# Performance work log

Measured on AMD Instinct MI355X. Metric: run time of the kernel, lower is better.

The kernel has to match this reference:

```python
import jax, jax.numpy as jnp
import numpy as np

MAX_CAV = 5


def setup_inputs() -> dict:
    key = jax.random.key(0)
    k1, k2, k3, k4, k5 = jax.random.split(key, 5)
    # ragged group lengths, each <= MAX_CAV, sum = 25
    record_len = jnp.array([3, 5, 2, 4, 1, 5, 3, 2], dtype=jnp.int32)
    N, C, H, W = 25, 256, 48, 176
    x = jax.random.normal(k1, (N, C, H, W), dtype=jnp.float32)
    W1 = jax.random.normal(k2, (MAX_CAV, 2 * MAX_CAV), dtype=jnp.float32) * 0.3
    W2 = jax.random.normal(k3, (MAX_CAV, MAX_CAV), dtype=jnp.float32) * 0.3
    conv_w = jax.random.normal(k4, (MAX_CAV,), dtype=jnp.float32) * 0.3
    conv_b = jax.random.normal(k5, (1,), dtype=jnp.float32) * 0.1
    return dict(x=x, record_len=record_len, W1=W1, W2=W2, conv_w=conv_w, conv_b=conv_b)


def _pad_regroup(x, record_len, max_cav):
    # scatter ragged tokens into a zero-padded [bs, max_cav, C, H, W] buffer
    N = x.shape[0]
    bs = record_len.shape[0]
    cum = jnp.cumsum(record_len)
    tok = jnp.arange(N)
    b = jnp.searchsorted(cum, tok, side='right')      # batch id per token
    slot = tok - (cum[b] - record_len[b])             # position within group
    padded = jnp.zeros((bs, max_cav) + x.shape[1:], x.dtype)
    return padded.at[b, slot].set(x)


def reference(x, record_len, W1, W2, conv_w, conv_b):
    padded = _pad_regroup(x, record_len, MAX_CAV)     # [bs, M, C, H, W]
    # AdaptiveAvg/MaxPool3d(1) over (C,H,W); padded slots are all-zero -> max=0
    x_avg = padded.mean(axis=(2, 3, 4))               # [bs, M]
    x_max = padded.max(axis=(2, 3, 4))                # [bs, M]
    x_sq = jnp.concatenate([x_avg, x_max], axis=1)    # [bs, 2M]
    gate = jax.nn.relu(jax.nn.sigmoid(x_sq @ W1.T) @ W2.T)  # [bs, M]
    scaled = padded * gate[:, :, None, None, None]
    # 1x1x1 Conv3d(M -> 1) == weighted sum over CAV axis + bias, then ReLU
    out = jax.nn.relu(jnp.einsum('m,bmchw->bchw', conv_w, scaled) + conv_b[0])
    return out
```

## Files before the change

### kernel.cpp

```cpp
#include <hip/hip_runtime.h>
#include <math.h>

#define CHW     2162688
#define V4      540672
#define NTOK    25
#define MAXCAV  5
#define NBATCH  8

#define BPT     64
#define V4_BLK  8448
#define ITERS   33

#define ABLKS   1056
#define CHUNK3  512

typedef float f32x4 __attribute__((ext_vector_type(4)));

__global__ __launch_bounds__(256) void k_reduce(const float4* __restrict__ x,
                                                float* __restrict__ psum,
                                                float* __restrict__ pmax) {
    const int tid = threadIdx.x;
    const int t   = blockIdx.y;
    const int blk = blockIdx.x;
    const long base = (long)t * V4 + (long)blk * V4_BLK;

    float s = 0.0f;
    float mx = -INFINITY;
    #pragma unroll 4
    for (int i = 0; i < ITERS; ++i) {
        float4 v = x[base + i * 256 + tid];
        s += (v.x + v.y) + (v.z + v.w);
        mx = fmaxf(mx, fmaxf(fmaxf(v.x, v.y), fmaxf(v.z, v.w)));
    }

    const int lane = tid & 63;
    const int wave = tid >> 6;
    #pragma unroll
    for (int off = 32; off > 0; off >>= 1) {
        s += __shfl_xor(s, off, 64);
        mx = fmaxf(mx, __shfl_xor(mx, off, 64));
    }
    __shared__ float rs[4], rm[4];
    if (lane == 0) { rs[wave] = s; rm[wave] = mx; }
    __syncthreads();
    if (tid == 0) {
        psum[t * BPT + blk] = rs[0] + rs[1] + rs[2] + rs[3];
        pmax[t * BPT + blk] = fmaxf(fmaxf(rm[0], rm[1]), fmaxf(rm[2], rm[3]));
    }
}

__global__ __launch_bounds__(256) void k_gate(const float* __restrict__ psum,
                                              const float* __restrict__ pmax,
                                              const int*   __restrict__ record_len,
                                              const float* __restrict__ W1,
                                              const float* __restrict__ W2,
                                              const float* __restrict__ conv_w,
                                              float* __restrict__ tok_coef,
                                              int*   __restrict__ tok_end)
{
    __shared__ float tsum[NTOK], tmax[NTOK];
    __shared__ float scoef[NBATCH][MAXCAV];
    __shared__ int   sstart[NBATCH], slen[NBATCH];
    const int wave = threadIdx.x >> 6;
    const int lane = threadIdx.x & 63;
    const int tid  = threadIdx.x;

    for (int t = wave; t < NTOK; t += 4) {
        float s = psum[t * BPT + lane];
        float m = pmax[t * BPT + lane];
        #pragma unroll
        for (int off = 32; off > 0; off >>= 1) {
            s += __shfl_xor(s, off, 64);
            m = fmaxf(m, __shfl_xor(m, off, 64));
        }
        if (lane == 0) { tsum[t] = s; tmax[t] = m; }
    }
    __syncthreads();

    if (tid < NBATCH) {
        const int b = tid;
        int start = 0;
        for (int i = 0; i < b; ++i) start += record_len[i];
        const int len = record_len[b];
        sstart[b] = start;
        slen[b]   = len;

        float xsq[2 * MAXCAV];
        #pragma unroll
        for (int m = 0; m < MAXCAV; ++m) {
            const bool valid = m < len;
            xsq[m]          = valid ? tsum[start + m] * (1.0f / (float)CHW) : 0.0f;
            xsq[MAXCAV + m] = valid ? tmax[start + m] : 0.0f;
        }
        float h[MAXCAV];
        #pragma unroll
        for (int j = 0; j < MAXCAV; ++j) {
            float a = 0.0f;
            #pragma unroll
            for (int k = 0; k < 2 * MAXCAV; ++k) a += xsq[k] * W1[j * 2 * MAXCAV + k];
            h[j] = 1.0f / (1.0f + expf(-a));
        }
        #pragma unroll
        for (int m = 0; m < MAXCAV; ++m) {
            float g = 0.0f;
            #pragma unroll
            for (int j = 0; j < MAXCAV; ++j) g += h[j] * W2[m * MAXCAV + j];
            scoef[b][m] = conv_w[m] * fmaxf(g, 0.0f);
        }
    }
    __syncthreads();

    if (tid < NTOK) {
        int b = 0;
        #pragma unroll
        for (int i = 0; i < NBATCH; ++i)
            if (tid >= sstart[i] + slen[i]) b = i + 1;
        const int m = tid - sstart[b];
        tok_coef[tid] = scoef[b][m];
        tok_end[tid]  = (m == slen[b] - 1) ? b : -1;
    }
}

__device__ __forceinline__ void relu_store(f32x4 a, float4* __restrict__ out, int o) {
    f32x4 acc;
    acc.x = fmaxf(a.x, 0.0f);
    acc.y = fmaxf(a.y, 0.0f);
    acc.z = fmaxf(a.z, 0.0f);
    acc.w = fmaxf(a.w, 0.0f);
    __builtin_nontemporal_store(acc, (f32x4*)(out + o));
}

__global__ __launch_bounds__(256) void k_apply(const float4* __restrict__ x,
                                               const float* __restrict__ tok_coef,
                                               const int*   __restrict__ tok_end,
                                               const float* __restrict__ conv_b,
                                               float4* __restrict__ out) {
    const int tid = threadIdx.x;
    const int idx = blockIdx.x * CHUNK3 + tid;
    const float bias = conv_b[0];

    float tc[NTOK];
    int   te[NTOK];
    #pragma unroll
    for (int t = 0; t < NTOK; ++t) { tc[t] = tok_coef[t]; te[t] = tok_end[t]; }

    f32x4 a0, a1;
    a0.x = a0.y = a0.z = a0.w = bias;
    a1 = a0;

    #pragma unroll
    for (int t = 0; t < NTOK; ++t) {
        const float4 v0 = x[t * V4 + idx];
        const float4 v1 = x[t * V4 + idx + 256];
        const float c = tc[t];
        a0.x += c * v0.x;  a0.y += c * v0.y;  a0.z += c * v0.z;  a0.w += c * v0.w;
        a1.x += c * v1.x;  a1.y += c * v1.y;  a1.z += c * v1.z;  a1.w += c * v1.w;
        if (te[t] >= 0) {
            const int obase = te[t] * V4 + idx;
            relu_store(a0, out, obase);
            relu_store(a1, out, obase + 256);
            a0.x = a0.y = a0.z = a0.w = bias;
            a1 = a0;
        }
    }
}

extern "C" void kernel_launch(void* const* d_in, const int* in_sizes, int n_in,
                              void* d_out, int out_size, void* d_ws, size_t ws_size,
                              hipStream_t stream) {
    const float4* x  = (const float4*)d_in[0];
    const int*    rl = (const int*)d_in[1];
    const float*  W1 = (const float*)d_in[2];
    const float*  W2 = (const float*)d_in[3];
    const float*  cw = (const float*)d_in[4];
    const float*  cb = (const float*)d_in[5];
    float4* out = (float4*)d_out;

    char* ws = (char*)d_ws;
    float* psum     = (float*)(ws);
    float* pmax     = (float*)(ws + 6400);
    float* tok_coef = (float*)(ws + 12800);
    int*   tok_end  = (int*)  (ws + 12800 + 128);

    k_reduce<<<dim3(BPT, NTOK), 256, 0, stream>>>(x, psum, pmax);
    k_gate<<<1, 256, 0, stream>>>(psum, pmax, rl, W1, W2, cw, tok_coef, tok_end);
    k_apply<<<ABLKS, 256, 0, stream>>>(x, tok_coef, tok_end, cb, out);
}
```

Before: 82.36 us.

## Flatten reduction grid into 2048 even chunks spanning token boundaries

The per-token 2D reduction grid (64 blocks per token, 1600 total) is replaced by a flat grid of 2048 equal chunks over the whole tensor. A chunk may straddle a token boundary, so each block keeps two partial sum/max pairs. The gate kernel then gathers each token's partials from the range of chunks that overlap it. The aim is an even block count across the GPU's compute units and less tail imbalance, at the cost of extra selects in straddling blocks and more complex indexing in the gate kernel.

```diff
diff --git a/kernel.cpp b/kernel.cpp
--- a/kernel.cpp
+++ b/kernel.cpp
@@ -7,9 +7,8 @@
 #define MAXCAV  5
 #define NBATCH  8
 
-#define BPT     64
-#define V4_BLK  8448
-#define ITERS   33
+#define RBLKS   2048
+#define CHUNK1  6600
 
 #define ABLKS   1056
 #define CHUNK3  512
@@ -17,40 +16,76 @@
 typedef float f32x4 __attribute__((ext_vector_type(4)));
 
 __global__ __launch_bounds__(256) void k_reduce(const float4* __restrict__ x,
-                                                float* __restrict__ psum,
-                                                float* __restrict__ pmax) {
-    const int tid = threadIdx.x;
-    const int t   = blockIdx.y;
-    const int blk = blockIdx.x;
-    const long base = (long)t * V4 + (long)blk * V4_BLK;
-
-    float s = 0.0f;
-    float mx = -INFINITY;
-    #pragma unroll 4
-    for (int i = 0; i < ITERS; ++i) {
-        float4 v = x[base + i * 256 + tid];
-        s += (v.x + v.y) + (v.z + v.w);
-        mx = fmaxf(mx, fmaxf(fmaxf(v.x, v.y), fmaxf(v.z, v.w)));
+                                                float* __restrict__ ps,
+                                                float* __restrict__ pm) {
+    const int tid   = threadIdx.x;
+    const int bid   = blockIdx.x;
+    const int base  = bid * CHUNK1;
+    const int t0    = base / V4;
+    const int split = min((t0 + 1) * V4 - base, CHUNK1);
+
+    float s0 = 0.f, s1 = 0.f, m0 = -INFINITY, m1 = -INFINITY;
+
+    if (split == CHUNK1) {
+        #pragma unroll 5
+        for (int i = 0; i < 25; ++i) {
+            float4 v = x[base + i * 256 + tid];
+            s0 += (v.x + v.y) + (v.z + v.w);
+            m0 = fmaxf(m0, fmaxf(fmaxf(v.x, v.y), fmaxf(v.z, v.w)));
+        }
+        if (tid < 200) {
+            float4 v = x[base + 6400 + tid];
+            s0 += (v.x + v.y) + (v.z + v.w);
+            m0 = fmaxf(m0, fmaxf(fmaxf(v.x, v.y), fmaxf(v.z, v.w)));
+        }
+    } else {
+        #pragma unroll 5
+        for (int i = 0; i < 25; ++i) {
+            const int li = i * 256 + tid;
+            float4 v = x[base + li];
+            const float vs = (v.x + v.y) + (v.z + v.w);
+            const float vm = fmaxf(fmaxf(v.x, v.y), fmaxf(v.z, v.w));
+            const bool first = li < split;
+            s0 += first ? vs : 0.f;
+            s1 += first ? 0.f : vs;
+            m0 = fmaxf(m0, first ? vm : -INFINITY);
+            m1 = fmaxf(m1, first ? -INFINITY : vm);
+        }
+        if (tid < 200) {
+            const int li = 6400 + tid;
+            float4 v = x[base + li];
+            const float vs = (v.x + v.y) + (v.z + v.w);
+            const float vm = fmaxf(fmaxf(v.x, v.y), fmaxf(v.z, v.w));
+            const bool first = li < split;
+            s0 += first ? vs : 0.f;
+            s1 += first ? 0.f : vs;
+            m0 = fmaxf(m0, first ? vm : -INFINITY);
+            m1 = fmaxf(m1, first ? -INFINITY : vm);
+        }
     }
 
     const int lane = tid & 63;
     const int wave = tid >> 6;
     #pragma unroll
     for (int off = 32; off > 0; off >>= 1) {
-        s += __shfl_xor(s, off, 64);
-        mx = fmaxf(mx, __shfl_xor(mx, off, 64));
-    }
-    __shared__ float rs[4], rm[4];
-    if (lane == 0) { rs[wave] = s; rm[wave] = mx; }
+        s0 += __shfl_xor(s0, off, 64);
+        s1 += __shfl_xor(s1, off, 64);
+        m0 = fmaxf(m0, __shfl_xor(m0, off, 64));
+        m1 = fmaxf(m1, __shfl_xor(m1, off, 64));
+    }
+    __shared__ float rs0[4], rs1[4], rm0[4], rm1[4];
+    if (lane == 0) { rs0[wave] = s0; rs1[wave] = s1; rm0[wave] = m0; rm1[wave] = m1; }
     __syncthreads();
     if (tid == 0) {
-        psum[t * BPT + blk] = rs[0] + rs[1] + rs[2] + rs[3];
-        pmax[t * BPT + blk] = fmaxf(fmaxf(rm[0], rm[1]), fmaxf(rm[2], rm[3]));
-    }
-}
-
-__global__ __launch_bounds__(256) void k_gate(const float* __restrict__ psum,
-                                              const float* __restrict__ pmax,
+        ps[2 * bid]     = rs0[0] + rs0[1] + rs0[2] + rs0[3];
+        ps[2 * bid + 1] = rs1[0] + rs1[1] + rs1[2] + rs1[3];
+        pm[2 * bid]     = fmaxf(fmaxf(rm0[0], rm0[1]), fmaxf(rm0[2], rm0[3]));
+        pm[2 * bid + 1] = fmaxf(fmaxf(rm1[0], rm1[1]), fmaxf(rm1[2], rm1[3]));
+    }
+}
+
+__global__ __launch_bounds__(256) void k_gate(const float* __restrict__ ps,
+                                              const float* __restrict__ pm,
                                               const int*   __restrict__ record_len,
                                               const float* __restrict__ W1,
                                               const float* __restrict__ W2,
@@ -66,8 +101,14 @@
     const int tid  = threadIdx.x;
 
     for (int t = wave; t < NTOK; t += 4) {
-        float s = psum[t * BPT + lane];
-        float m = pmax[t * BPT + lane];
+        const int b_lo = (t == 0) ? 0 : ((t - 1) * V4 + CHUNK1 - 1) / CHUNK1;
+        const int b_hi = min(RBLKS - 1, ((t + 1) * V4 + CHUNK1 - 1) / CHUNK1 - 1);
+        float s = 0.f, m = -INFINITY;
+        for (int b = b_lo + lane; b <= b_hi; b += 64) {
+            const int tb = (b * CHUNK1) / V4;
+            if (tb == t)     { s += ps[2 * b];     m = fmaxf(m, pm[2 * b]); }
+            if (tb == t - 1) { s += ps[2 * b + 1]; m = fmaxf(m, pm[2 * b + 1]); }
+        }
         #pragma unroll
         for (int off = 32; off > 0; off >>= 1) {
             s += __shfl_xor(s, off, 64);
@@ -177,12 +218,12 @@
     float4* out = (float4*)d_out;
 
     char* ws = (char*)d_ws;
-    float* psum     = (float*)(ws);
-    float* pmax     = (float*)(ws + 6400);
-    float* tok_coef = (float*)(ws + 12800);
-    int*   tok_end  = (int*)  (ws + 12800 + 128);
-
-    k_reduce<<<dim3(BPT, NTOK), 256, 0, stream>>>(x, psum, pmax);
-    k_gate<<<1, 256, 0, stream>>>(psum, pmax, rl, W1, W2, cw, tok_coef, tok_end);
+    float* ps       = (float*)(ws);
+    float* pm       = (float*)(ws + 16384);
+    float* tok_coef = (float*)(ws + 32768);
+    int*   tok_end  = (int*)  (ws + 32768 + 128);
+
+    k_reduce<<<RBLKS, 256, 0, stream>>>(x, ps, pm);
+    k_gate<<<1, 256, 0, stream>>>(ps, pm, rl, W1, W2, cw, tok_coef, tok_end);
     k_apply<<<ABLKS, 256, 0, stream>>>(x, tok_coef, tok_end, cb, out);
 }
```

Result: slower. 87.35 us (+6.1%).
